# Kernel optimization log

Hardware: AMD Instinct MI355X
Metric: run time of the kernel (lower is better)

## Reference

```python
import jax, jax.numpy as jnp
import numpy as np

N = 500000   # num_nodes
K = 32       # ring buffer slots (max_neighbors)
B = 8192     # event batch size
D = 128      # memory_dim == embedding_dim == attention input_dim
T = 64       # time_dim
H = 2        # num_heads
KS = 16      # top-k sampled neighbors per query


def time_encode(dt, w, b):
    # Time2Vec: sin on even channels, cos on odd channels. dt [...], w/b [T]
    f = dt[..., None] * w + b
    even = (jnp.arange(w.shape[0]) % 2) == 0
    return jnp.where(even, jnp.sin(f), jnp.cos(f))


def setup_inputs() -> dict:
    key = jax.random.key(0)
    ks = jax.random.split(key, 40)
    def rn(i, shape, s=0.05):
        return jax.random.normal(ks[i], shape, dtype=jnp.float32) * s
    inp = {}
    inp["src"] = jax.random.randint(ks[0], (B,), 0, N)
    inp["dst"] = jax.random.randint(ks[1], (B,), 0, N)
    # shift query timestamps so every row has valid (earlier) neighbors w.h.p.
    inp["ts"] = 0.5 + 0.5 * jax.random.uniform(ks[2], (B,), dtype=jnp.float32)
    inp["nbr_ids"] = jax.random.randint(ks[3], (N, K), 0, N, dtype=jnp.int32)
    inp["nbr_ts"] = jax.random.uniform(ks[4], (N, K), dtype=jnp.float32)
    inp["memory"] = rn(5, (N, D), 0.1)
    inp["last_update"] = jnp.zeros((N,), jnp.float32)
    # message function: TimeEncoding + MLP(2*D + T -> D -> D)
    inp["w_t_msg"] = rn(6, (T,), 0.1); inp["b_t_msg"] = jnp.zeros((T,), jnp.float32)
    inp["W_msg1"] = rn(7, (D, 2 * D + T)); inp["b_msg1"] = jnp.zeros((D,), jnp.float32)
    inp["W_msg2"] = rn(8, (D, D)); inp["b_msg2"] = jnp.zeros((D,), jnp.float32)
    # GRUCell(message_dim=D, memory_dim=D)
    inp["W_ih"] = rn(9, (3 * D, D)); inp["b_ih"] = jnp.zeros((3 * D,), jnp.float32)
    inp["W_hh"] = rn(10, (3 * D, D)); inp["b_hh"] = jnp.zeros((3 * D,), jnp.float32)
    # temporal attention
    inp["w_t_att"] = rn(11, (T,), 0.1); inp["b_t_att"] = jnp.zeros((T,), jnp.float32)
    inp["Wq"] = rn(12, (D, D)); inp["bq"] = jnp.zeros((D,), jnp.float32)
    inp["Wk"] = rn(13, (D, D + T)); inp["bk"] = jnp.zeros((D,), jnp.float32)
    inp["Wv"] = rn(14, (D, D + T)); inp["bv"] = jnp.zeros((D,), jnp.float32)
    inp["Wo"] = rn(15, (D, D)); inp["bo"] = jnp.zeros((D,), jnp.float32)
    # merge MLP(D + D -> D -> D) + layernorm
    inp["Wm1"] = rn(16, (D, 2 * D)); inp["bm1"] = jnp.zeros((D,), jnp.float32)
    inp["Wm2"] = rn(17, (D, D)); inp["bm2"] = jnp.zeros((D,), jnp.float32)
    inp["ln_g"] = jnp.ones((D,), jnp.float32); inp["ln_b"] = jnp.zeros((D,), jnp.float32)
    return inp


def reference(src, dst, ts, nbr_ids, nbr_ts, memory, last_update,
              w_t_msg, b_t_msg, W_msg1, b_msg1, W_msg2, b_msg2,
              W_ih, b_ih, W_hh, b_hh,
              w_t_att, b_t_att, Wq, bq, Wk, bk, Wv, bv, Wo, bo,
              Wm1, bm1, Wm2, bm2, ln_g, ln_b):
    # ---- C1: message computation + GRU memory scatter-update (both endpoints) ----
    nodes = jnp.concatenate([src, dst])        # [2B]
    others = jnp.concatenate([dst, src])
    tb = jnp.concatenate([ts, ts])
    self_mem = memory[nodes]                   # [2B, D] gather
    oth_mem = memory[others]
    dt = tb - last_update[nodes]
    te = time_encode(dt, w_t_msg, b_t_msg)     # [2B, T]
    x = jnp.concatenate([self_mem, oth_mem, te], axis=-1)
    msg = jax.nn.relu(x @ W_msg1.T + b_msg1) @ W_msg2.T + b_msg2   # [2B, D]
    # GRUCell
    gi = msg @ W_ih.T + b_ih
    gh = self_mem @ W_hh.T + b_hh
    ir, iz, ig = jnp.split(gi, 3, axis=-1)
    hr, hz, hg = jnp.split(gh, 3, axis=-1)
    r = jax.nn.sigmoid(ir + hr)
    z = jax.nn.sigmoid(iz + hz)
    g = jnp.tanh(ig + r * hg)
    new_mem = (1.0 - z) * g + z * self_mem
    mem2 = memory.at[nodes].set(new_mem)       # scatter-update

    # ---- temporal top-k neighbor sampling for src queries ----
    ids = nbr_ids[src]                         # [B, K]
    nts = nbr_ts[src]                          # [B, K]
    valid = (ids >= 0) & (nts < ts[:, None] + 1e-6)
    sort_ts = jnp.where(valid, nts, -1e30)
    _, idx = jax.lax.top_k(sort_ts, KS)        # most recent first
    sel_ids = jnp.take_along_axis(ids, idx, axis=1)
    sel_ts = jnp.take_along_axis(nts, idx, axis=1)
    mk = jnp.take_along_axis(valid, idx, axis=1)
    tdelta = jnp.where(mk, ts[:, None] - sel_ts, 0.0)
    sel_ids = jnp.clip(jnp.where(mk, sel_ids, 0), 0, N - 1)

    # ---- temporal attention embedding layer ----
    nbr_feat = mem2[sel_ids]                   # [B, KS, D] gather
    node_feat = mem2[src]                      # [B, D]
    te_a = time_encode(tdelta, w_t_att, b_t_att)        # [B, KS, T]
    kv = jnp.concatenate([nbr_feat, te_a], axis=-1)     # [B, KS, D+T]
    hd = D // H
    Q = (node_feat @ Wq.T + bq).reshape(B, H, hd)
    Kp = (kv @ Wk.T + bk).reshape(B, KS, H, hd).transpose(0, 2, 1, 3)
    Vp = (kv @ Wv.T + bv).reshape(B, KS, H, hd).transpose(0, 2, 1, 3)
    scores = jnp.einsum('bhd,bhnd->bhn', Q, Kp) / jnp.sqrt(jnp.float32(hd))
    scores = jnp.where(mk[:, None, :], scores, -jnp.inf)
    attn = jnp.nan_to_num(jax.nn.softmax(scores, axis=-1), nan=0.0)
    out = jnp.einsum('bhn,bhnd->bhd', attn, Vp).reshape(B, D)
    attn_out = out @ Wo.T + bo
    # merge with memory + layernorm
    comb = jnp.concatenate([attn_out, node_feat], axis=-1)
    h = jax.nn.relu(comb @ Wm1.T + bm1) @ Wm2.T + bm2
    mu = h.mean(axis=-1, keepdims=True)
    var = ((h - mu) ** 2).mean(axis=-1, keepdims=True)
    emb = (h - mu) / jnp.sqrt(var + 1e-5) * ln_g + ln_b   # [B, D]
    return emb
```

## Files before the change

### kernel.cpp

```cpp
#include <hip/hip_runtime.h>
#include <math.h>

#define BATCH  8192
#define NNODES 500000
#define DIM    128
#define TDIM   64
#define KNB    32
#define KSEL   16

#define OFF_W1   0
#define OFF_W2   40960
#define OFF_WIH  57344
#define OFF_WHH  106496
#define OFF_WQ   155648
#define OFF_WV   172032
#define OFF_WO   196608
#define OFF_WM1  212992
#define OFF_WM2  245760
#define OFF_WKT  262144
#define CVT_TOT  286720

#define NB_CVT  1120

typedef float  f32x4  __attribute__((ext_vector_type(4)));
typedef __bf16 bf16x8 __attribute__((ext_vector_type(8)));
typedef short  s16x8  __attribute__((ext_vector_type(8)));

#define MFMA(a,b,c) __builtin_amdgcn_mfma_f32_16x16x32_bf16(a,b,c,0,0,0)

__device__ __forceinline__ float rcpf_(float x) { return __builtin_amdgcn_rcpf(x); }
__device__ __forceinline__ float fsigmoid(float x) { return rcpf_(1.f + __expf(-x)); }
__device__ __forceinline__ float ftanh(float x) {
    float e = __expf(2.f * x);
    return 1.f - 2.f * rcpf_(e + 1.f);
}
__device__ __forceinline__ unsigned short f2bf(float x) {
    unsigned u = __builtin_bit_cast(unsigned, x);
    unsigned r = (u + 0x7FFFu + ((u >> 16) & 1u)) >> 16;
    return (unsigned short)r;
}
__device__ __forceinline__ float bf2f(unsigned short u) {
    unsigned v = ((unsigned)u) << 16;
    return __builtin_bit_cast(float, v);
}
__device__ __forceinline__ bf16x8 ldfrag(const unsigned short* p) {
    s16x8 v = *(const s16x8*)p;
    return __builtin_bit_cast(bf16x8, v);
}
__device__ __forceinline__ uint2 pack4bf(float4 v) {
    uint2 pk;
    pk.x = (unsigned)f2bf(v.x) | ((unsigned)f2bf(v.y) << 16);
    pk.y = (unsigned)f2bf(v.z) | ((unsigned)f2bf(v.w) << 16);
    return pk;
}

__global__ __launch_bounds__(256) void k_prep(
    const float* __restrict__ sW1, const float* __restrict__ sW2,
    const float* __restrict__ sWih, const float* __restrict__ sWhh,
    const float* __restrict__ sWq, const float* __restrict__ sWv,
    const float* __restrict__ sWo, const float* __restrict__ sWm1,
    const float* __restrict__ sWm2, const float* __restrict__ sWk,
    unsigned short* __restrict__ pool,
    int* __restrict__ winner)
{
    const int i = blockIdx.x * 256 + threadIdx.x;
    {
        float v;
        if      (i < OFF_W2)  { v = sW1 [i - OFF_W1 ]; }
        else if (i < OFF_WIH) { v = sW2 [i - OFF_W2 ]; }
        else if (i < OFF_WHH) { v = sWih[i - OFF_WIH]; }
        else if (i < OFF_WQ)  { v = sWhh[i - OFF_WHH]; }
        else if (i < OFF_WV)  { v = sWq [i - OFF_WQ ]; }
        else if (i < OFF_WO)  { v = sWv [i - OFF_WV ]; }
        else if (i < OFF_WM1) { v = sWo [i - OFF_WO ]; }
        else if (i < OFF_WM2) { v = sWm1[i - OFF_WM1]; }
        else if (i < OFF_WKT) { v = sWm2[i - OFF_WM2]; }
        else {
            int j = i - OFF_WKT;
            int h = j / 12288, rem = j % 12288;
            int c = rem >> 6, dh = rem & 63;
            v = sWk[(size_t)(h * 64 + dh) * 192 + c];
        }
        pool[i] = f2bf(v);
    }
    for (int j = i; j < NNODES; j += NB_CVT * 256) winner[j] = -1;
}

__global__ __launch_bounds__(512) void k1_mfma(
    const int* __restrict__ src, const int* __restrict__ dst, const float* __restrict__ ts,
    const float* __restrict__ memory, const float* __restrict__ last_update,
    const float* __restrict__ w_t, const float* __restrict__ b_t,
    const unsigned short* __restrict__ Wp,
    const float* __restrict__ b1, const float* __restrict__ b2,
    const float* __restrict__ bih, const float* __restrict__ bhh,
    float* __restrict__ new_mem,
    int* __restrict__ winner,
    const int* __restrict__ nbr_ids, const float* __restrict__ nbr_ts,
    int* __restrict__ sel_id, float* __restrict__ sel_td, int* __restrict__ sel_mk)
{
    __shared__ unsigned short sxb[64][328];
    __shared__ unsigned short hb [64][136];
    __shared__ int   s_node[64];
    __shared__ int   s_oth [64];
    __shared__ float s_dt  [64];

    const unsigned short* W1b  = Wp + OFF_W1;
    const unsigned short* W2b  = Wp + OFF_W2;
    const unsigned short* Wihb = Wp + OFF_WIH;
    const unsigned short* Whhb = Wp + OFF_WHH;

    const int tid  = threadIdx.x;
    const int bid  = blockIdx.x;
    const int base = bid * 64;

    if (tid < 64) {
        int i = bid * 64 + tid;
        int v = (i < BATCH) ? src[i] : dst[i - BATCH];
        atomicMax(&winner[v], i);
    }
    {
        const int w = tid >> 6, l = tid & 63;
        const int j = l & 31;
        int   bq0 = bid * 32 + w * 4 + (l >> 5);
        int   bq1 = bq0 + 2;
        int   s0 = src[bq0], s1 = src[bq1];
        float t0 = ts[bq0],  t1 = ts[bq1];
        int   id0 = nbr_ids[(size_t)s0 * KNB + j];
        float nt0 = nbr_ts [(size_t)s0 * KNB + j];
        int   id1 = nbr_ids[(size_t)s1 * KNB + j];
        float nt1 = nbr_ts [(size_t)s1 * KNB + j];
        {
            bool valid = (id0 >= 0) && (nt0 < t0 + 1e-6f);
            float key = valid ? nt0 : -1e30f;
            int rank = 0;
            #pragma unroll
            for (int m = 0; m < 32; ++m) {
                float ok = __shfl(key, (l & 32) + m);
                rank += (ok > key) || (ok == key && m < j);
            }
            if (rank < KSEL) {
                int oid = id0 < 0 ? 0 : (id0 > NNODES - 1 ? NNODES - 1 : id0);
                sel_id[bq0 * KSEL + rank] = valid ? oid : 0;
                sel_td[bq0 * KSEL + rank] = valid ? (t0 - nt0) : 0.f;
                sel_mk[bq0 * KSEL + rank] = valid ? 1 : 0;
            }
        }
        {
            bool valid = (id1 >= 0) && (nt1 < t1 + 1e-6f);
            float key = valid ? nt1 : -1e30f;
            int rank = 0;
            #pragma unroll
            for (int m = 0; m < 32; ++m) {
                float ok = __shfl(key, (l & 32) + m);
                rank += (ok > key) || (ok == key && m < j);
            }
            if (rank < KSEL) {
                int oid = id1 < 0 ? 0 : (id1 > NNODES - 1 ? NNODES - 1 : id1);
                sel_id[bq1 * KSEL + rank] = valid ? oid : 0;
                sel_td[bq1 * KSEL + rank] = valid ? (t1 - nt1) : 0.f;
                sel_mk[bq1 * KSEL + rank] = valid ? 1 : 0;
            }
        }
    }

    if (tid < 64) {
        int gi = base + tid;
        int node, oth; float t;
        if (gi < BATCH) { node = src[gi];         oth = dst[gi];         t = ts[gi]; }
        else            { node = dst[gi - BATCH]; oth = src[gi - BATCH]; t = ts[gi - BATCH]; }
        s_node[tid] = node;
        s_oth[tid]  = oth;
        s_dt[tid]   = t - last_update[node];
    }
    __syncthreads();

    for (int idx = tid; idx < 64 * 32; idx += 512) {
        int r = idx >> 5, c4 = (idx & 31) << 2;
        float4 vs = *(const float4*)&memory[(size_t)s_node[r] * DIM + c4];
        float4 vo = *(const float4*)&memory[(size_t)s_oth[r]  * DIM + c4];
        *(uint2*)&sxb[r][c4]       = pack4bf(vs);
        *(uint2*)&sxb[r][128 + c4] = pack4bf(vo);
    }
    for (int idx = tid; idx < 64 * TDIM; idx += 512) {
        int r = idx >> 6, c = idx & 63;
        float f = s_dt[r] * w_t[c] + b_t[c];
        sxb[r][256 + c] = f2bf((c & 1) ? __cosf(f) : __sinf(f));
    }
    __syncthreads();

    const int w    = tid >> 6;
    const int l    = tid & 63;
    const int rowA = l & 15;
    const int kg   = l >> 4;
    const int n0   = w * 16;
    const int col  = l & 15;
    const int rgrp = l >> 4;

    {
        f32x4 a0 = {0.f,0.f,0.f,0.f}, a1 = {0.f,0.f,0.f,0.f};
        f32x4 a2 = {0.f,0.f,0.f,0.f}, a3 = {0.f,0.f,0.f,0.f};
        #pragma unroll
        for (int kt = 0; kt < 10; ++kt) {
            int ko = kt * 32 + kg * 8;
            bf16x8 bfr = ldfrag(&W1b[(size_t)(n0 + rowA) * 320 + ko]);
            a0 = MFMA(ldfrag(&sxb[     rowA][ko]), bfr, a0);
            a1 = MFMA(ldfrag(&sxb[16 + rowA][ko]), bfr, a1);
            a2 = MFMA(ldfrag(&sxb[32 + rowA][ko]), bfr, a2);
            a3 = MFMA(ldfrag(&sxb[48 + rowA][ko]), bfr, a3);
        }
        float bb = b1[n0 + col];
        #pragma unroll
        for (int rgi = 0; rgi < 4; ++rgi) {
            int rb = rgrp * 4 + rgi;
            hb[rb     ][n0 + col] = f2bf(fmaxf(a0[rgi] + bb, 0.f));
            hb[rb + 16][n0 + col] = f2bf(fmaxf(a1[rgi] + bb, 0.f));
            hb[rb + 32][n0 + col] = f2bf(fmaxf(a2[rgi] + bb, 0.f));
            hb[rb + 48][n0 + col] = f2bf(fmaxf(a3[rgi] + bb, 0.f));
        }
    }
    __syncthreads();

    {
        f32x4 m0 = {0.f,0.f,0.f,0.f}, m1 = {0.f,0.f,0.f,0.f};
        f32x4 m2 = {0.f,0.f,0.f,0.f}, m3 = {0.f,0.f,0.f,0.f};
        #pragma unroll
        for (int kt = 0; kt < 4; ++kt) {
            int ko = kt * 32 + kg * 8;
            bf16x8 bfr = ldfrag(&W2b[(size_t)(n0 + rowA) * 128 + ko]);
            m0 = MFMA(ldfrag(&hb[     rowA][ko]), bfr, m0);
            m1 = MFMA(ldfrag(&hb[16 + rowA][ko]), bfr, m1);
            m2 = MFMA(ldfrag(&hb[32 + rowA][ko]), bfr, m2);
            m3 = MFMA(ldfrag(&hb[48 + rowA][ko]), bfr, m3);
        }
        __syncthreads();
        float bb = b2[n0 + col];
        #pragma unroll
        for (int rgi = 0; rgi < 4; ++rgi) {
            int rb = rgrp * 4 + rgi;
            hb[rb     ][n0 + col] = f2bf(m0[rgi] + bb);
            hb[rb + 16][n0 + col] = f2bf(m1[rgi] + bb);
            hb[rb + 32][n0 + col] = f2bf(m2[rgi] + bb);
            hb[rb + 48][n0 + col] = f2bf(m3[rgi] + bb);
        }
    }
    __syncthreads();

    {
        f32x4 g[6][4];
        #pragma unroll
        for (int gi_ = 0; gi_ < 6; ++gi_)
            #pragma unroll
            for (int ta = 0; ta < 4; ++ta) g[gi_][ta] = (f32x4){0.f,0.f,0.f,0.f};
        #pragma unroll
        for (int kt = 0; kt < 4; ++kt) {
            int ko = kt * 32 + kg * 8;
            int br = n0 + rowA;
            bf16x8 bir = ldfrag(&Wihb[(size_t)(      br) * 128 + ko]);
            bf16x8 biz = ldfrag(&Wihb[(size_t)(128 + br) * 128 + ko]);
            bf16x8 big = ldfrag(&Wihb[(size_t)(256 + br) * 128 + ko]);
            bf16x8 bhr = ldfrag(&Whhb[(size_t)(      br) * 128 + ko]);
            bf16x8 bhz = ldfrag(&Whhb[(size_t)(128 + br) * 128 + ko]);
            bf16x8 bhg = ldfrag(&Whhb[(size_t)(256 + br) * 128 + ko]);
            #pragma unroll
            for (int ta = 0; ta < 4; ++ta) {
                bf16x8 am = ldfrag(&hb [ta * 16 + rowA][ko]);
                bf16x8 ah = ldfrag(&sxb[ta * 16 + rowA][ko]);
                g[0][ta] = MFMA(am, bir, g[0][ta]);
                g[1][ta] = MFMA(am, biz, g[1][ta]);
                g[2][ta] = MFMA(am, big, g[2][ta]);
                g[3][ta] = MFMA(ah, bhr, g[3][ta]);
                g[4][ta] = MFMA(ah, bhz, g[4][ta]);
                g[5][ta] = MFMA(ah, bhg, g[5][ta]);
            }
        }
        const int d = n0 + col;
        float bir = bih[d], biz = bih[128 + d], big = bih[256 + d];
        float bhr = bhh[d], bhz = bhh[128 + d], bhg = bhh[256 + d];
        #pragma unroll
        for (int ta = 0; ta < 4; ++ta)
            #pragma unroll
            for (int rgi = 0; rgi < 4; ++rgi) {
                int rr = ta * 16 + rgrp * 4 + rgi;
                float rv = fsigmoid((g[0][ta][rgi] + bir) + (g[3][ta][rgi] + bhr));
                float zv = fsigmoid((g[1][ta][rgi] + biz) + (g[4][ta][rgi] + bhz));
                float gv = ftanh((g[2][ta][rgi] + big) + rv * (g[5][ta][rgi] + bhg));
                float selfv = bf2f(sxb[rr][d]);
                new_mem[(size_t)(base + rr) * DIM + d] = (1.f - zv) * gv + zv * selfv;
            }
    }
}

__global__ __launch_bounds__(512) void k3_fused(
    const int* __restrict__ src,
    const float* __restrict__ memory, const float* __restrict__ new_mem,
    const int* __restrict__ winner,
    const int* __restrict__ sel_id, const float* __restrict__ sel_td,
    const int* __restrict__ sel_mk,
    const float* __restrict__ w_ta, const float* __restrict__ b_ta,
    const unsigned short* __restrict__ Wp,
    const float* __restrict__ bq, const float* __restrict__ bk,
    const float* __restrict__ bv, const float* __restrict__ bo,
    const float* __restrict__ bm1, const float* __restrict__ bm2,
    const float* __restrict__ ln_g, const float* __restrict__ ln_b,
    float* __restrict__ out)
{
    __shared__ unsigned short s_nfB[32][136];
    __shared__ unsigned short s_qB [32][136];
    __shared__ float          s_u  [32][2][200];
    __shared__ unsigned short s_kvb[32][2][200];
    __shared__ unsigned long long s_pool64[6400];
    __shared__ const float* s_nptr[32][16];
    __shared__ float s_td [32][16];
    __shared__ int   s_mk [32][16];
    __shared__ float s_qb [32][2];
    __shared__ float s_satt[32][2];
    __shared__ float s_at [8][2][16];
    __shared__ const float* s_ptr[32];

    const unsigned short* Wqb  = Wp + OFF_WQ;
    const unsigned short* WkTb = Wp + OFF_WKT;
    const unsigned short* Wvb  = Wp + OFF_WV;
    const unsigned short* Wob  = Wp + OFF_WO;
    const unsigned short* Wm1b = Wp + OFF_WM1;
    const unsigned short* Wm2b = Wp + OFF_WM2;

    const int tid  = threadIdx.x;
    const int base = blockIdx.x * 32;

    if (tid < 32) {
        int v = src[base + tid];
        int wv = winner[v];
        s_ptr[tid] = (wv >= 0) ? (new_mem + (size_t)wv * DIM)
                               : (memory  + (size_t)v  * DIM);
    }
    {
        int r = tid >> 4, n = tid & 15;
        int id = sel_id[(base + r) * KSEL + n];
        int wi = winner[id];
        s_nptr[r][n] = (wi >= 0) ? (new_mem + (size_t)wi * DIM)
                                 : (memory  + (size_t)id * DIM);
        s_td[r][n] = sel_td[(base + r) * KSEL + n];
        s_mk[r][n] = sel_mk[(base + r) * KSEL + n];
    }
    __syncthreads();

    for (int idx = tid; idx < 32 * 32; idx += 512) {
        int r = idx >> 5, c4 = (idx & 31) << 2;
        float4 v = *(const float4*)&s_ptr[r][c4];
        *(uint2*)&s_nfB[r][c4] = pack4bf(v);
    }
    __syncthreads();

    const int w    = tid >> 6;
    const int l    = tid & 63;
    const int rowA = l & 15;
    const int kg   = l >> 4;
    const int col  = l & 15;
    const int rgrp = l >> 4;

    {
        const int n0 = w * 16;
        f32x4 q0 = {0.f,0.f,0.f,0.f}, q1 = {0.f,0.f,0.f,0.f};
        #pragma unroll
        for (int kt = 0; kt < 4; ++kt) {
            int ko = kt * 32 + kg * 8;
            bf16x8 bfr = ldfrag(&Wqb[(size_t)(n0 + rowA) * 128 + ko]);
            q0 = MFMA(ldfrag(&s_nfB[     rowA][ko]), bfr, q0);
            q1 = MFMA(ldfrag(&s_nfB[16 + rowA][ko]), bfr, q1);
        }
        float bb = bq[n0 + col];
        #pragma unroll
        for (int rgi = 0; rgi < 4; ++rgi) {
            int rb = rgrp * 4 + rgi;
            s_qB[rb     ][n0 + col] = f2bf(q0[rgi] + bb);
            s_qB[rb + 16][n0 + col] = f2bf(q1[rgi] + bb);
        }
    }
    __syncthreads();

    if (tid < 256) {
        int r = tid >> 3, rem = tid & 7, h = rem >> 2, p = rem & 3;
        float part = 0.f;
        #pragma unroll
        for (int j = 0; j < 16; ++j) {
            int dd = h * 64 + p * 16 + j;
            part += bf2f(s_qB[r][dd]) * bk[dd];
        }
        part += __shfl_xor(part, 1);
        part += __shfl_xor(part, 2);
        if (p == 0) s_qb[r][h] = part;
    }

    {
        const int h  = w >> 2;
        const int cb = (w & 3) * 48;
        f32x4 u[3][2];
        #pragma unroll
        for (int ct = 0; ct < 3; ++ct)
            #pragma unroll
            for (int ta = 0; ta < 2; ++ta) u[ct][ta] = (f32x4){0.f,0.f,0.f,0.f};
        #pragma unroll
        for (int kt = 0; kt < 2; ++kt) {
            int ko = kt * 32 + kg * 8;
            bf16x8 bfr[3];
            #pragma unroll
            for (int ct = 0; ct < 3; ++ct)
                bfr[ct] = ldfrag(&WkTb[(size_t)h * 12288 + (size_t)(cb + ct * 16 + rowA) * 64 + ko]);
            #pragma unroll
            for (int ta = 0; ta < 2; ++ta) {
                bf16x8 av = ldfrag(&s_qB[ta * 16 + rowA][h * 64 + ko]);
                #pragma unroll
                for (int ct = 0; ct < 3; ++ct)
                    u[ct][ta] = MFMA(av, bfr[ct], u[ct][ta]);
            }
        }
        #pragma unroll
        for (int ct = 0; ct < 3; ++ct)
            #pragma unroll
            for (int ta = 0; ta < 2; ++ta)
                #pragma unroll
                for (int rgi = 0; rgi < 4; ++rgi) {
                    int rr = ta * 16 + rgrp * 4 + rgi;
                    s_u[rr][h][cb + ct * 16 + col] = u[ct][ta][rgi];
                }
    }
    __syncthreads();

    {
        unsigned short (*kvbuf)[16][200] = (unsigned short (*)[16][200])s_pool64;
        float wt = w_ta[l], bt = b_ta[l];
        const int pfn = l >> 5;
        const int pfc = (l & 31) << 2;

        float4 pf[8];
        {
            const int r = w * 4;
            #pragma unroll
            for (int it = 0; it < 8; ++it)
                pf[it] = *(const float4*)&s_nptr[r][it * 2 + pfn][pfc];
        }

        for (int rr = 0; rr < 4; ++rr) {
            const int r = w * 4 + rr;
            #pragma unroll
            for (int it = 0; it < 8; ++it)
                *(uint2*)&kvbuf[w][it * 2 + pfn][pfc] = pack4bf(pf[it]);
            #pragma unroll
            for (int n = 0; n < 16; ++n) {
                float f = s_td[r][n] * wt + bt;
                kvbuf[w][n][128 + l] = f2bf((l & 1) ? __cosf(f) : __sinf(f));
            }
            if (rr < 3) {
                const int rn = r + 1;
                #pragma unroll
                for (int it = 0; it < 8; ++it)
                    pf[it] = *(const float4*)&s_nptr[rn][it * 2 + pfn][pfc];
            }
            __builtin_amdgcn_wave_barrier();

            {
                int h = (l >> 4) & 1, n = l & 15, half = l >> 5;
                float acc = (half == 0) ? s_qb[r][h] : 0.f;
                const unsigned short* kvrow = &kvbuf[w][n][half * 96];
                const float* urow = &s_u[r][h][half * 96];
                #pragma unroll
                for (int k = 0; k < 96; k += 8) {
                    s16x8 kv8 = *(const s16x8*)&kvrow[k];
                    #pragma unroll
                    for (int j = 0; j < 8; ++j)
                        acc += bf2f((unsigned short)kv8[j]) * urow[k + j];
                }
                acc += __shfl_xor(acc, 32);
                int mk = s_mk[r][n];
                float s = mk ? acc * 0.125f : -INFINITY;
                float mx = s;
                #pragma unroll
                for (int m = 1; m < 16; m <<= 1) mx = fmaxf(mx, __shfl_xor(mx, m));
                float p = (mk && mx > -1e37f) ? __expf(s - mx) : 0.f;
                float den = p;
                #pragma unroll
                for (int m = 1; m < 16; m <<= 1) den += __shfl_xor(den, m);
                float a = (den > 0.f) ? (p * rcpf_(den)) : 0.f;
                if (l < 32) s_at[w][h][n] = a;
                if (l == 0 || l == 16) s_satt[r][h] = (den > 0.f) ? 1.f : 0.f;
            }
            __builtin_amdgcn_wave_barrier();

            #pragma unroll
            for (int i = 0; i < 3; ++i) {
                int c = i * 64 + l;
                float k0 = 0.f, k1 = 0.f;
                #pragma unroll
                for (int n = 0; n < 16; ++n) {
                    float v = bf2f(kvbuf[w][n][c]);
                    k0 += s_at[w][0][n] * v;
                    k1 += s_at[w][1][n] * v;
                }
                s_kvb[r][0][c] = f2bf(k0);
                s_kvb[r][1][c] = f2bf(k1);
            }
            __builtin_amdgcn_wave_barrier();
        }
    }
    __syncthreads();

    unsigned short (*s_aoB)[136] = (unsigned short (*)[136])s_pool64;
    unsigned short (*s_oB )[136] = (unsigned short (*)[136])((char*)s_pool64 + 8704);
    unsigned short (*s_h1B)[136] = (unsigned short (*)[136])((char*)s_pool64 + 17408);
    float          (*s_h2 )[128] = (float          (*)[128])((char*)s_pool64 + 26112);

    {
        const int h  = w >> 2;
        const int c0 = (w & 3) * 16;
        f32x4 o0 = {0.f,0.f,0.f,0.f}, o1 = {0.f,0.f,0.f,0.f};
        #pragma unroll
        for (int kt = 0; kt < 6; ++kt) {
            int ko = kt * 32 + kg * 8;
            bf16x8 bfr = ldfrag(&Wvb[(size_t)(h * 64 + c0 + rowA) * 192 + ko]);
            o0 = MFMA(ldfrag(&s_kvb[     rowA][h][ko]), bfr, o0);
            o1 = MFMA(ldfrag(&s_kvb[16 + rowA][h][ko]), bfr, o1);
        }
        int d0 = h * 64 + c0 + col;
        float bv0 = bv[d0];
        #pragma unroll
        for (int rgi = 0; rgi < 4; ++rgi) {
            int rb = rgrp * 4 + rgi;
            s_oB[rb     ][d0] = f2bf(o0[rgi] + s_satt[rb     ][h] * bv0);
            s_oB[rb + 16][d0] = f2bf(o1[rgi] + s_satt[rb + 16][h] * bv0);
        }
    }
    __syncthreads();

    {
        const int n0 = w * 16;
        f32x4 a0 = {0.f,0.f,0.f,0.f}, a1 = {0.f,0.f,0.f,0.f};
        #pragma unroll
        for (int kt = 0; kt < 4; ++kt) {
            int ko = kt * 32 + kg * 8;
            bf16x8 bfr = ldfrag(&Wob[(size_t)(n0 + rowA) * 128 + ko]);
            a0 = MFMA(ldfrag(&s_oB[     rowA][ko]), bfr, a0);
            a1 = MFMA(ldfrag(&s_oB[16 + rowA][ko]), bfr, a1);
        }
        float bb = bo[n0 + col];
        #pragma unroll
        for (int rgi = 0; rgi < 4; ++rgi) {
            int rb = rgrp * 4 + rgi;
            s_aoB[rb     ][n0 + col] = f2bf(a0[rgi] + bb);
            s_aoB[rb + 16][n0 + col] = f2bf(a1[rgi] + bb);
        }
    }
    __syncthreads();

    {
        const int n0 = w * 16;
        f32x4 a0 = {0.f,0.f,0.f,0.f}, a1 = {0.f,0.f,0.f,0.f};
        #pragma unroll
        for (int kt = 0; kt < 8; ++kt) {
            int ko = kt * 32 + kg * 8;
            bf16x8 av0 = (kt < 4) ? ldfrag(&s_aoB[     rowA][ko])
                                  : ldfrag(&s_nfB[     rowA][ko - 128]);
            bf16x8 av1 = (kt < 4) ? ldfrag(&s_aoB[16 + rowA][ko])
                                  : ldfrag(&s_nfB[16 + rowA][ko - 128]);
            bf16x8 bfr = ldfrag(&Wm1b[(size_t)(n0 + rowA) * 256 + ko]);
            a0 = MFMA(av0, bfr, a0);
            a1 = MFMA(av1, bfr, a1);
        }
        float bb = bm1[n0 + col];
        #pragma unroll
        for (int rgi = 0; rgi < 4; ++rgi) {
            int rb = rgrp * 4 + rgi;
            s_h1B[rb     ][n0 + col] = f2bf(fmaxf(a0[rgi] + bb, 0.f));
            s_h1B[rb + 16][n0 + col] = f2bf(fmaxf(a1[rgi] + bb, 0.f));
        }
    }
    __syncthreads();

    {
        const int n0 = w * 16;
        f32x4 a0 = {0.f,0.f,0.f,0.f}, a1 = {0.f,0.f,0.f,0.f};
        #pragma unroll
        for (int kt = 0; kt < 4; ++kt) {
            int ko = kt * 32 + kg * 8;
            bf16x8 bfr = ldfrag(&Wm2b[(size_t)(n0 + rowA) * 128 + ko]);
            a0 = MFMA(ldfrag(&s_h1B[     rowA][ko]), bfr, a0);
            a1 = MFMA(ldfrag(&s_h1B[16 + rowA][ko]), bfr, a1);
        }
        float bb = bm2[n0 + col];
        #pragma unroll
        for (int rgi = 0; rgi < 4; ++rgi) {
            int rb = rgrp * 4 + rgi;
            s_h2[rb     ][n0 + col] = a0[rgi] + bb;
            s_h2[rb + 16][n0 + col] = a1[rgi] + bb;
        }
    }
    __syncthreads();

    {
        float lg0 = ln_g[l], lg1 = ln_g[64 + l];
        float lb0 = ln_b[l], lb1 = ln_b[64 + l];
        #pragma unroll
        for (int i = 0; i < 4; ++i) {
            int r = w * 4 + i;
            float v0 = s_h2[r][l], v1 = s_h2[r][64 + l];
            float sum = v0 + v1;
            #pragma unroll
            for (int m = 1; m < 64; m <<= 1) sum += __shfl_xor(sum, m);
            float mean = sum * (1.f / 128.f);
            float e0 = v0 - mean, e1 = v1 - mean;
            float sq = e0 * e0 + e1 * e1;
            #pragma unroll
            for (int m = 1; m < 64; m <<= 1) sq += __shfl_xor(sq, m);
            float inv = rsqrtf(sq * (1.f / 128.f) + 1e-5f);
            out[(size_t)(base + r) * DIM + l]      = e0 * inv * lg0 + lb0;
            out[(size_t)(base + r) * DIM + 64 + l] = e1 * inv * lg1 + lb1;
        }
    }
}

extern "C" void kernel_launch(void* const* d_in, const int* in_sizes, int n_in,
                              void* d_out, int out_size, void* d_ws, size_t ws_size,
                              hipStream_t stream) {
    const int*   src         = (const int*)  d_in[0];
    const int*   dst         = (const int*)  d_in[1];
    const float* ts          = (const float*)d_in[2];
    const int*   nbr_ids     = (const int*)  d_in[3];
    const float* nbr_ts      = (const float*)d_in[4];
    const float* memory      = (const float*)d_in[5];
    const float* last_update = (const float*)d_in[6];
    const float* w_t_msg     = (const float*)d_in[7];
    const float* b_t_msg     = (const float*)d_in[8];
    const float* W_msg1      = (const float*)d_in[9];
    const float* b_msg1      = (const float*)d_in[10];
    const float* W_msg2      = (const float*)d_in[11];
    const float* b_msg2      = (const float*)d_in[12];
    const float* W_ih        = (const float*)d_in[13];
    const float* b_ih        = (const float*)d_in[14];
    const float* W_hh        = (const float*)d_in[15];
    const float* b_hh        = (const float*)d_in[16];
    const float* w_t_att     = (const float*)d_in[17];
    const float* b_t_att     = (const float*)d_in[18];
    const float* Wq          = (const float*)d_in[19];
    const float* bq          = (const float*)d_in[20];
    const float* Wk          = (const float*)d_in[21];
    const float* bk          = (const float*)d_in[22];
    const float* Wv          = (const float*)d_in[23];
    const float* bv          = (const float*)d_in[24];
    const float* Wo          = (const float*)d_in[25];
    const float* bo          = (const float*)d_in[26];
    const float* Wm1         = (const float*)d_in[27];
    const float* bm1         = (const float*)d_in[28];
    const float* Wm2         = (const float*)d_in[29];
    const float* bm2         = (const float*)d_in[30];
    const float* ln_g        = (const float*)d_in[31];
    const float* ln_b        = (const float*)d_in[32];
    float* out = (float*)d_out;

    char* ws = (char*)d_ws;
    size_t off = 0;
    float* new_mem = (float*)(ws + off); off += (size_t)2 * BATCH * DIM * 4;
    int*   winner  = (int*)  (ws + off); off += 2097152;
    int*   sel_id  = (int*)  (ws + off); off += (size_t)BATCH * KSEL * 4;
    float* sel_td  = (float*)(ws + off); off += (size_t)BATCH * KSEL * 4;
    int*   sel_mk  = (int*)  (ws + off); off += (size_t)BATCH * KSEL * 4;
    unsigned short* Wpool = (unsigned short*)(ws + off); off += (size_t)CVT_TOT * 2;

    k_prep<<<NB_CVT, 256, 0, stream>>>(
        W_msg1, W_msg2, W_ih, W_hh, Wq, Wv, Wo, Wm1, Wm2, Wk, Wpool, winner);
    k1_mfma<<<(2 * BATCH) / 64, 512, 0, stream>>>(
        src, dst, ts, memory, last_update,
        w_t_msg, b_t_msg, Wpool, b_msg1, b_msg2, b_ih, b_hh, new_mem,
        winner, nbr_ids, nbr_ts, sel_id, sel_td, sel_mk);
    k3_fused<<<BATCH / 32, 512, 0, stream>>>(
        src, memory, new_mem, winner, sel_id, sel_td, sel_mk,
        w_t_att, b_t_att, Wpool, bq, bk, bv, bo, bm1, bm2, ln_g, ln_b, out);
}
```

Measured before the change: 62.49 us.

## Prefetch memory gathers into registers early and vectorize attention-weighted sum

In k1, the memory row gathers for src/dst are now issued at kernel start into registers, before the atomic winner update and neighbor top-k selection. The aim is to hide global-memory latency behind that work and to drop the shared index arrays and one barrier. In k2, the node feature gather computes its pointers inline without the s_ptr barrier, and the neighbor-row prefetch is hoisted before the Q projection. The attention-weighted KV sum now processes bf16 pairs with 32-bit LDS loads and stores. These changes raise register pressure, which may reduce occupancy.

Result: faster. 60.26 us (-3.6%).

```diff
diff --git a/kernel.cpp b/kernel.cpp
--- a/kernel.cpp
+++ b/kernel.cpp
@@ -100,9 +100,7 @@
 {
     __shared__ unsigned short sxb[64][328];
     __shared__ unsigned short hb [64][136];
-    __shared__ int   s_node[64];
-    __shared__ int   s_oth [64];
-    __shared__ float s_dt  [64];
+    __shared__ float s_dt[64];
 
     const unsigned short* W1b  = Wp + OFF_W1;
     const unsigned short* W2b  = Wp + OFF_W2;
@@ -112,6 +110,19 @@
     const int tid  = threadIdx.x;
     const int bid  = blockIdx.x;
     const int base = bid * 64;
+
+    float4 vs[4], vo[4];
+    #pragma unroll
+    for (int k = 0; k < 4; ++k) {
+        int idx = tid + k * 512;
+        int r = idx >> 5, c4 = (idx & 31) << 2;
+        int gi = base + r;
+        bool isrc = gi < BATCH;
+        int node = isrc ? src[gi] : dst[gi - BATCH];
+        int oth  = isrc ? dst[gi] : src[gi - BATCH];
+        vs[k] = *(const float4*)&memory[(size_t)node * DIM + c4];
+        vo[k] = *(const float4*)&memory[(size_t)oth  * DIM + c4];
+    }
 
     if (tid < 64) {
         int i = bid * 64 + tid;
@@ -165,22 +176,21 @@
 
     if (tid < 64) {
         int gi = base + tid;
-        int node, oth; float t;
-        if (gi < BATCH) { node = src[gi];         oth = dst[gi];         t = ts[gi]; }
-        else            { node = dst[gi - BATCH]; oth = src[gi - BATCH]; t = ts[gi - BATCH]; }
-        s_node[tid] = node;
-        s_oth[tid]  = oth;
-        s_dt[tid]   = t - last_update[node];
-    }
-    __syncthreads();
-
-    for (int idx = tid; idx < 64 * 32; idx += 512) {
+        bool isrc = gi < BATCH;
+        int node = isrc ? src[gi] : dst[gi - BATCH];
+        float t  = isrc ? ts[gi]  : ts[gi - BATCH];
+        s_dt[tid] = t - last_update[node];
+    }
+
+    #pragma unroll
+    for (int k = 0; k < 4; ++k) {
+        int idx = tid + k * 512;
         int r = idx >> 5, c4 = (idx & 31) << 2;
-        float4 vs = *(const float4*)&memory[(size_t)s_node[r] * DIM + c4];
-        float4 vo = *(const float4*)&memory[(size_t)s_oth[r]  * DIM + c4];
-        *(uint2*)&sxb[r][c4]       = pack4bf(vs);
-        *(uint2*)&sxb[r][128 + c4] = pack4bf(vo);
-    }
+        *(uint2*)&sxb[r][c4]       = pack4bf(vs[k]);
+        *(uint2*)&sxb[r][128 + c4] = pack4bf(vo[k]);
+    }
+    __syncthreads();
+
     for (int idx = tid; idx < 64 * TDIM; idx += 512) {
         int r = idx >> 6, c = idx & 63;
         float f = s_dt[r] * w_t[c] + b_t[c];
@@ -315,7 +325,6 @@
     __shared__ float s_qb [32][2];
     __shared__ float s_satt[32][2];
     __shared__ float s_at [8][2][16];
-    __shared__ const float* s_ptr[32];
 
     const unsigned short* Wqb  = Wp + OFF_WQ;
     const unsigned short* WkTb = Wp + OFF_WKT;
@@ -327,12 +336,6 @@
     const int tid  = threadIdx.x;
     const int base = blockIdx.x * 32;
 
-    if (tid < 32) {
-        int v = src[base + tid];
-        int wv = winner[v];
-        s_ptr[tid] = (wv >= 0) ? (new_mem + (size_t)wv * DIM)
-                               : (memory  + (size_t)v  * DIM);
-    }
     {
         int r = tid >> 4, n = tid & 15;
         int id = sel_id[(base + r) * KSEL + n];
@@ -342,12 +345,17 @@
         s_td[r][n] = sel_td[(base + r) * KSEL + n];
         s_mk[r][n] = sel_mk[(base + r) * KSEL + n];
     }
-    __syncthreads();
-
-    for (int idx = tid; idx < 32 * 32; idx += 512) {
+
+    #pragma unroll
+    for (int k = 0; k < 2; ++k) {
+        int idx = tid + k * 512;
         int r = idx >> 5, c4 = (idx & 31) << 2;
-        float4 v = *(const float4*)&s_ptr[r][c4];
-        *(uint2*)&s_nfB[r][c4] = pack4bf(v);
+        int v = src[base + r];
+        int wv = winner[v];
+        const float* p = (wv >= 0) ? (new_mem + (size_t)wv * DIM)
+                                   : (memory  + (size_t)v  * DIM);
+        float4 val = *(const float4*)&p[c4];
+        *(uint2*)&s_nfB[r][c4] = pack4bf(val);
     }
     __syncthreads();
 
@@ -358,6 +366,16 @@
     const int col  = l & 15;
     const int rgrp = l >> 4;
 
+    const int pfn = l >> 5;
+    const int pfc = (l & 31) << 2;
+    float4 pf[8];
+    {
+        const int r = w * 4;
+        #pragma unroll
+        for (int it = 0; it < 8; ++it)
+            pf[it] = *(const float4*)&s_nptr[r][it * 2 + pfn][pfc];
+    }
+
     {
         const int n0 = w * 16;
         f32x4 q0 = {0.f,0.f,0.f,0.f}, q1 = {0.f,0.f,0.f,0.f};
@@ -429,16 +447,6 @@
     {
         unsigned short (*kvbuf)[16][200] = (unsigned short (*)[16][200])s_pool64;
         float wt = w_ta[l], bt = b_ta[l];
-        const int pfn = l >> 5;
-        const int pfc = (l & 31) << 2;
-
-        float4 pf[8];
-        {
-            const int r = w * 4;
-            #pragma unroll
-            for (int it = 0; it < 8; ++it)
-                pf[it] = *(const float4*)&s_nptr[r][it * 2 + pfn][pfc];
-        }
 
         for (int rr = 0; rr < 4; ++rr) {
             const int r = w * 4 + rr;
@@ -487,17 +495,24 @@
             __builtin_amdgcn_wave_barrier();
 
             #pragma unroll
-            for (int i = 0; i < 3; ++i) {
-                int c = i * 64 + l;
-                float k0 = 0.f, k1 = 0.f;
-                #pragma unroll
-                for (int n = 0; n < 16; ++n) {
-                    float v = bf2f(kvbuf[w][n][c]);
-                    k0 += s_at[w][0][n] * v;
-                    k1 += s_at[w][1][n] * v;
+            for (int ps = 0; ps < 2; ++ps) {
+                int cp = (ps == 0) ? l : (64 + l);
+                if (!(ps == 1 && l >= 32)) {
+                    float ke0 = 0.f, ke1 = 0.f, ko0 = 0.f, ko1 = 0.f;
+                    #pragma unroll
+                    for (int n = 0; n < 16; ++n) {
+                        unsigned pv = *(const unsigned*)&kvbuf[w][n][cp * 2];
+                        float ve = bf2f((unsigned short)(pv & 0xFFFFu));
+                        float vd = bf2f((unsigned short)(pv >> 16));
+                        float a0 = s_at[w][0][n], a1 = s_at[w][1][n];
+                        ke0 += a0 * ve; ke1 += a1 * ve;
+                        ko0 += a0 * vd; ko1 += a1 * vd;
+                    }
+                    unsigned o0 = (unsigned)f2bf(ke0) | ((unsigned)f2bf(ko0) << 16);
+                    unsigned o1 = (unsigned)f2bf(ke1) | ((unsigned)f2bf(ko1) << 16);
+                    *(unsigned*)&s_kvb[r][0][cp * 2] = o0;
+                    *(unsigned*)&s_kvb[r][1][cp * 2] = o1;
                 }
-                s_kvb[r][0][c] = f2bf(k0);
-                s_kvb[r][1][c] = f2bf(k1);
             }
             __builtin_amdgcn_wave_barrier();
         }
```
